# Kernel tuning notes

Hardware: AMD Instinct MI355X
Metric: run time of the kernel (lower is better)

Reference implementation:

```python
import jax, jax.numpy as jnp
import numpy as np

NUM_NODES = 100000
EMBED_DIM = 64
NUM_EDGES = 1200000
NUM_LAYERS = 3
ALPHA = 0.25  # 1 / (num_layers + 1)


def setup_inputs() -> dict:
    key = jax.random.key(0)
    k1, k2, k3, k4 = jax.random.split(key, 4)
    x = jax.random.normal(k1, (NUM_NODES, EMBED_DIM), dtype=jnp.float32)
    edge_attr = jax.random.uniform(k2, (NUM_EDGES,), dtype=jnp.float32)
    edge_index = jax.random.randint(k3, (2, NUM_EDGES), 0, NUM_NODES, dtype=jnp.int64)
    edge_mask = jax.random.randint(k4, (NUM_EDGES,), 0, 2, dtype=jnp.int32).astype(jnp.bool_)
    return {"x": x, "edge_attr": edge_attr, "edge_index": edge_index, "edge_mask": edge_mask}


def reference(x, edge_attr, edge_index, edge_mask):
    # Masked edge selection == zeroing masked edge weights (same degree & aggregation).
    w = edge_attr * edge_mask.astype(edge_attr.dtype)  # [E]
    row, col = edge_index[0], edge_index[1]            # source, target

    # gcn_norm with add_self_loops=False: D^{-1/2} A D^{-1/2}
    deg = jax.ops.segment_sum(w, col, num_segments=NUM_NODES)          # [N]
    dinv = jnp.where(deg > 0, jax.lax.rsqrt(deg), 0.0)                 # [N]
    norm = dinv[row] * w * dinv[col]                                   # [E]

    out = ALPHA * x
    h = x
    for _ in range(NUM_LAYERS):
        msg = norm[:, None] * h[row]                                   # [E, D] gather
        h = jax.ops.segment_sum(msg, col, num_segments=NUM_NODES)      # [N, D] scatter
        out = out + ALPHA * h
    return out
```

## Files before the change

kernel.cpp:

```cpp
#include <hip/hip_runtime.h>
#include <hip/hip_fp16.h>

#define N_NODES 100000
#define EMB     64
#define N_EDGES 1200000
#define ALPHA   0.25f
#define SCAN_CHUNK 1024
#define NPART ((N_NODES + SCAN_CHUNK - 1) / SCAN_CHUNK)

__global__ void k_detect(const unsigned char* __restrict__ maskB,
                         const int* __restrict__ idx, int* __restrict__ flags) {
    int tid = blockIdx.x * blockDim.x + threadIdx.x;
    int lane = threadIdx.x & 63;
    bool mev = (tid & 3) && maskB[tid];
    if (__any(mev) && lane == 0) atomicOr(&flags[0], 1);
    bool iev = (tid < 4096) && (idx[2 * tid + 1] != 0);
    if (__any(iev) && lane == 0) atomicOr(&flags[1], 1);
}

__device__ __forceinline__ int idx_row(const int* idx, int i64, int e) {
    return i64 ? idx[2 * e] : idx[e];
}
__device__ __forceinline__ int idx_col(const int* idx, int i64, int e) {
    return i64 ? idx[2 * (N_EDGES + e)] : idx[N_EDGES + e];
}
__device__ __forceinline__ int edge_mask(const void* maskp, int mbool, int e) {
    return mbool ? (int)((const unsigned char*)maskp)[e] : ((const int*)maskp)[e];
}

__global__ void k_hist(const float* __restrict__ ea, const void* maskp,
                       const int* __restrict__ idx, const int* __restrict__ flags,
                       int* __restrict__ cnt, int* __restrict__ rank) {
    int e = blockIdx.x * blockDim.x + threadIdx.x;
    if (e >= N_EDGES) return;
    int mbool = flags[0] != 0, i64 = (flags[1] == 0);
    if (!edge_mask(maskp, mbool, e)) return;
    float wv = ea[e];
    if (wv == 0.0f) return;
    int c = idx_col(idx, i64, e);
    if ((unsigned)c >= N_NODES) return;
    rank[e] = atomicAdd(&cnt[c], 1);
}

__global__ void k_scanx(const int* __restrict__ cnt, int* __restrict__ gTotal,
                        int* __restrict__ row_start) {
    __shared__ int sh[256];
    __shared__ int sbase;
    int tid = threadIdx.x;
    int base = blockIdx.x * SCAN_CHUNK + tid * 4;
    int v[4];
    int s = 0;
#pragma unroll
    for (int k = 0; k < 4; ++k) {
        int i = base + k;
        v[k] = (i < N_NODES) ? cnt[i] : 0;
        s += v[k];
    }
    sh[tid] = s;
    __syncthreads();
    for (int d = 1; d < 256; d <<= 1) {
        int t = (tid >= d) ? sh[tid - d] : 0;
        __syncthreads();
        sh[tid] += t;
        __syncthreads();
    }
    if (tid == 255) sbase = atomicAdd(gTotal, sh[255]);
    __syncthreads();
    int off = sbase + sh[tid] - s;
#pragma unroll
    for (int k = 0; k < 4; ++k) {
        int i = base + k;
        if (i < N_NODES) { row_start[i] = off; off += v[k]; }
    }
}

__global__ void k_fill(const float* __restrict__ ea, const void* maskp,
                       const int* __restrict__ idx, const int* __restrict__ flags,
                       const int* __restrict__ row_start, const int* __restrict__ rank,
                       int2* __restrict__ csr) {
    int e = blockIdx.x * blockDim.x + threadIdx.x;
    if (e >= N_EDGES) return;
    int mbool = flags[0] != 0, i64 = (flags[1] == 0);
    if (!edge_mask(maskp, mbool, e)) return;
    float wv = ea[e];
    if (wv == 0.0f) return;
    int c = idx_col(idx, i64, e);
    if ((unsigned)c >= N_NODES) return;
    int r = idx_row(idx, i64, e);
    int rok = (unsigned)r < N_NODES;
    int p = row_start[c] + rank[e];
    if ((unsigned)p < N_EDGES)
        csr[p] = make_int2(__float_as_int(rok ? wv : 0.0f), rok ? r : 0);
}

__device__ __forceinline__ void slice_bounds(const int* row_start, const int* cnt,
                                             int n, int& beg, int& end) {
    beg = row_start[n];
    if (beg < 0) beg = 0;
    if (beg > N_EDGES) beg = N_EDGES;
    int c = cnt[n];
    if (c < 0) c = 0;
    end = beg + c;
    if (end > N_EDGES) end = N_EDGES;
}

__global__ __launch_bounds__(256) void k_degconv(
        const int* __restrict__ row_start, const int* __restrict__ cnt,
        const int2* __restrict__ csr, const float4* __restrict__ x4,
        float4* __restrict__ t0, float* __restrict__ dinv, float* __restrict__ sd) {
    int t = blockIdx.x * blockDim.x + threadIdx.x;
    int n = t >> 3;
    int q = t & 7;
    if (n >= N_NODES) return;
    int beg, end;
    slice_bounds(row_start, cnt, n, beg, end);
    float s = 0.0f;
    for (int j = beg + q; j < end; j += 8) s += __int_as_float(csr[j].x);
    s += __shfl_xor(s, 1);
    s += __shfl_xor(s, 2);
    s += __shfl_xor(s, 4);
    float di = (s > 0.0f) ? rsqrtf(s) : 0.0f;
    if (q == 0) {
        dinv[n] = di;
        sd[n] = (s > 0.0f) ? sqrtf(s) : 0.0f;
    }
    size_t xb = (size_t)n * 16 + q * 2;
    float4 v0 = x4[xb], v1 = x4[xb + 1];
    float4 o;
    __half2* op = reinterpret_cast<__half2*>(&o);
    op[0] = __floats2half2_rn(di * v0.x, di * v0.y);
    op[1] = __floats2half2_rn(di * v0.z, di * v0.w);
    op[2] = __floats2half2_rn(di * v1.x, di * v1.y);
    op[3] = __floats2half2_rn(di * v1.z, di * v1.w);
    t0[(size_t)n * 8 + q] = o;
}

__device__ __forceinline__ void accum_h8(float4& sa, float4& sb, float w,
                                         float4 raw) {
    const __half2* hp = reinterpret_cast<const __half2*>(&raw);
    float2 f0 = __half22float2(hp[0]);
    float2 f1 = __half22float2(hp[1]);
    float2 f2 = __half22float2(hp[2]);
    float2 f3 = __half22float2(hp[3]);
    sa.x += w * f0.x; sa.y += w * f0.y; sa.z += w * f1.x; sa.w += w * f1.y;
    sb.x += w * f2.x; sb.y += w * f2.y; sb.z += w * f3.x; sb.w += w * f3.y;
}

__device__ __forceinline__ void gather_core_f16(
        const int* __restrict__ row_start, const int* __restrict__ cnt,
        const int2* __restrict__ csr, const float4* __restrict__ h16,
        int n, int q, float4& sa, float4& sb) {
    int beg, end;
    slice_bounds(row_start, cnt, n, beg, end);
    sa = make_float4(0.f, 0.f, 0.f, 0.f);
    sb = make_float4(0.f, 0.f, 0.f, 0.f);
    for (int j = beg; j < end; j += 4) {
        int last = end - 1;
        int j1 = j + 1 < last ? j + 1 : last;
        int j2 = j + 2 < last ? j + 2 : last;
        int j3 = j + 3 < last ? j + 3 : last;
        int2 p0 = csr[j];
        int2 p1 = csr[j1];
        int2 p2 = csr[j2];
        int2 p3 = csr[j3];
        bool a1 = j + 1 < end, a2 = j + 2 < end, a3 = j + 3 < end;
        float w0 = __int_as_float(p0.x);
        float w1 = a1 ? __int_as_float(p1.x) : 0.0f;
        float w2 = a2 ? __int_as_float(p2.x) : 0.0f;
        float w3 = a3 ? __int_as_float(p3.x) : 0.0f;
        int r0 = min((unsigned)p0.y, (unsigned)(N_NODES - 1));
        int r1 = a1 ? min((unsigned)p1.y, (unsigned)(N_NODES - 1)) : 0;
        int r2 = a2 ? min((unsigned)p2.y, (unsigned)(N_NODES - 1)) : 0;
        int r3 = a3 ? min((unsigned)p3.y, (unsigned)(N_NODES - 1)) : 0;
        float4 v0 = h16[(size_t)r0 * 8 + q];
        float4 v1 = h16[(size_t)r1 * 8 + q];
        float4 v2 = h16[(size_t)r2 * 8 + q];
        float4 v3 = h16[(size_t)r3 * 8 + q];
        accum_h8(sa, sb, w0, v0);
        accum_h8(sa, sb, w1, v1);
        accum_h8(sa, sb, w2, v2);
        accum_h8(sa, sb, w3, v3);
    }
}

__global__ __launch_bounds__(256) void k_gather_mid(
        const int* __restrict__ row_start, const int* __restrict__ cnt,
        const int2* __restrict__ csr, const float* __restrict__ dinv,
        const float4* __restrict__ tsrc, float4* __restrict__ tdst) {
    int t = blockIdx.x * blockDim.x + threadIdx.x;
    int n = t >> 3;
    int q = t & 7;
    if (n >= N_NODES) return;
    float4 sa, sb;
    gather_core_f16(row_start, cnt, csr, tsrc, n, q, sa, sb);
    float di = dinv[n];
    float d2 = di * di;
    float4 o;
    __half2* op = reinterpret_cast<__half2*>(&o);
    op[0] = __floats2half2_rn(d2 * sa.x, d2 * sa.y);
    op[1] = __floats2half2_rn(d2 * sa.z, d2 * sa.w);
    op[2] = __floats2half2_rn(d2 * sb.x, d2 * sb.y);
    op[3] = __floats2half2_rn(d2 * sb.z, d2 * sb.w);
    tdst[(size_t)n * 8 + q] = o;
}

__global__ __launch_bounds__(256) void k_gather_last(
        const int* __restrict__ row_start, const int* __restrict__ cnt,
        const int2* __restrict__ csr, const float* __restrict__ dinv,
        const float* __restrict__ sd,
        const float4* __restrict__ x4, const float4* __restrict__ t1_16,
        const float4* __restrict__ t2_16, float4* __restrict__ out4) {
    int t = blockIdx.x * blockDim.x + threadIdx.x;
    int n = t >> 3;
    int q = t & 7;
    if (n >= N_NODES) return;
    float4 sa, sb;
    gather_core_f16(row_start, cnt, csr, t2_16, n, q, sa, sb);
    float di = dinv[n];
    float sdv = sd[n];
    size_t o8 = (size_t)n * 8 + q;
    float4 r1 = t1_16[o8];
    float4 r2 = t2_16[o8];
    const __half2* a1 = reinterpret_cast<const __half2*>(&r1);
    const __half2* a2 = reinterpret_cast<const __half2*>(&r2);
    float2 b10 = __half22float2(a1[0]), b11 = __half22float2(a1[1]);
    float2 b12 = __half22float2(a1[2]), b13 = __half22float2(a1[3]);
    float2 b20 = __half22float2(a2[0]), b21 = __half22float2(a2[1]);
    float2 b22 = __half22float2(a2[2]), b23 = __half22float2(a2[3]);
    size_t ox = (size_t)n * 16 + 2 * q;
    float4 x0 = x4[ox], x1 = x4[ox + 1];
    float4 o0, o1;
    o0.x = ALPHA * (x0.x + sdv * (b10.x + b20.x) + di * sa.x);
    o0.y = ALPHA * (x0.y + sdv * (b10.y + b20.y) + di * sa.y);
    o0.z = ALPHA * (x0.z + sdv * (b11.x + b21.x) + di * sa.z);
    o0.w = ALPHA * (x0.w + sdv * (b11.y + b21.y) + di * sa.w);
    o1.x = ALPHA * (x1.x + sdv * (b12.x + b22.x) + di * sb.x);
    o1.y = ALPHA * (x1.y + sdv * (b12.y + b22.y) + di * sb.y);
    o1.z = ALPHA * (x1.z + sdv * (b13.x + b23.x) + di * sb.z);
    o1.w = ALPHA * (x1.w + sdv * (b13.y + b23.y) + di * sb.w);
    out4[ox] = o0;
    out4[ox + 1] = o1;
}

extern "C" void kernel_launch(void* const* d_in, const int* in_sizes, int n_in,
                              void* d_out, int out_size, void* d_ws, size_t ws_size,
                              hipStream_t stream) {
    const float* x   = (const float*)d_in[0];
    const float* ea  = (const float*)d_in[1];
    const int*   idx = (const int*)d_in[2];
    const void*  msk = d_in[3];
    float*       out = (float*)d_out;

    char* ws = (char*)d_ws;
    size_t off = 0;
    auto alloc = [&](size_t bytes) -> void* {
        void* p = ws + off;
        off = (off + bytes + 255) & ~(size_t)255;
        return p;
    };
    int*    flags     = (int*)   alloc(64);
    int*    cnt       = (int*)   alloc(sizeof(int)   * N_NODES);
    int*    row_start = (int*)   alloc(sizeof(int)   * N_NODES);
    float*  dinv      = (float*) alloc(sizeof(float) * N_NODES);
    float*  sd        = (float*) alloc(sizeof(float) * N_NODES);
    int*    rank      = (int*)   alloc(sizeof(int)   * N_EDGES);
    int2*   csr       = (int2*)  alloc(sizeof(int2)  * N_EDGES);
    float4* t0        = (float4*)alloc(sizeof(unsigned short) * (size_t)N_NODES * EMB);
    float4* tA        = (float4*)alloc(sizeof(unsigned short) * (size_t)N_NODES * EMB);
    float4* tB        = (float4*)alloc(sizeof(unsigned short) * (size_t)N_NODES * EMB);
    int*    gTotal    = flags + 8;

    const int B = 256;
    const int gE = (N_EDGES + B - 1) / B;
    const int gG = (N_NODES * 8 + B - 1) / B;

    (void)hipMemsetAsync(flags, 0, (size_t)((char*)row_start - (char*)flags), stream);
    k_detect <<<64, 256, 0, stream>>>((const unsigned char*)msk, idx, flags);
    k_hist   <<<gE, B, 0, stream>>>(ea, msk, idx, flags, cnt, rank);
    k_scanx  <<<NPART, 256, 0, stream>>>(cnt, gTotal, row_start);
    k_fill   <<<gE, B, 0, stream>>>(ea, msk, idx, flags, row_start, rank, csr);
    k_degconv<<<gG, B, 0, stream>>>(row_start, cnt, csr, (const float4*)x,
                                    t0, dinv, sd);

    k_gather_mid <<<gG, B, 0, stream>>>(row_start, cnt, csr, dinv, t0, tA);
    k_gather_mid <<<gG, B, 0, stream>>>(row_start, cnt, csr, dinv, tA, tB);
    k_gather_last<<<gG, B, 0, stream>>>(row_start, cnt, csr, dinv, sd,
                                        (const float4*)x, tA, tB, (float4*)out);
}
```

Measured before the change: 191.8 us.

## Replace per-edge rank array with atomic cursors and widen gather unroll to 8

The fill kernel now claims CSR slots with an atomic increment on a per-node cursor initialised by the scan. This removes the per-edge rank array write and read, and the histogram no longer returns atomic results. Zeroing of the count array moves from a memset into the detect kernel. The gather loop now loads 8 edges per iteration instead of 4 to keep more loads in flight. The cost is a second pass of contended atomics in fill, nondeterministic edge order within each row, and higher register pressure in the gather.

```diff
diff --git a/kernel.cpp b/kernel.cpp
--- a/kernel.cpp
+++ b/kernel.cpp
@@ -9,13 +9,15 @@
 #define NPART ((N_NODES + SCAN_CHUNK - 1) / SCAN_CHUNK)
 
 __global__ void k_detect(const unsigned char* __restrict__ maskB,
-                         const int* __restrict__ idx, int* __restrict__ flags) {
+                         const int* __restrict__ idx, int* __restrict__ flags,
+                         int* __restrict__ cnt) {
     int tid = blockIdx.x * blockDim.x + threadIdx.x;
     int lane = threadIdx.x & 63;
     bool mev = (tid & 3) && maskB[tid];
     if (__any(mev) && lane == 0) atomicOr(&flags[0], 1);
     bool iev = (tid < 4096) && (idx[2 * tid + 1] != 0);
     if (__any(iev) && lane == 0) atomicOr(&flags[1], 1);
+    for (int i = tid; i < N_NODES; i += 64 * 256) cnt[i] = 0;
 }
 
 __device__ __forceinline__ int idx_row(const int* idx, int i64, int e) {
@@ -30,7 +32,7 @@
 
 __global__ void k_hist(const float* __restrict__ ea, const void* maskp,
                        const int* __restrict__ idx, const int* __restrict__ flags,
-                       int* __restrict__ cnt, int* __restrict__ rank) {
+                       int* __restrict__ cnt) {
     int e = blockIdx.x * blockDim.x + threadIdx.x;
     if (e >= N_EDGES) return;
     int mbool = flags[0] != 0, i64 = (flags[1] == 0);
@@ -39,11 +41,11 @@
     if (wv == 0.0f) return;
     int c = idx_col(idx, i64, e);
     if ((unsigned)c >= N_NODES) return;
-    rank[e] = atomicAdd(&cnt[c], 1);
+    atomicAdd(&cnt[c], 1);
 }
 
 __global__ void k_scanx(const int* __restrict__ cnt, int* __restrict__ gTotal,
-                        int* __restrict__ row_start) {
+                        int* __restrict__ row_start, int* __restrict__ cursor) {
     __shared__ int sh[256];
     __shared__ int sbase;
     int tid = threadIdx.x;
@@ -70,14 +72,13 @@
 #pragma unroll
     for (int k = 0; k < 4; ++k) {
         int i = base + k;
-        if (i < N_NODES) { row_start[i] = off; off += v[k]; }
+        if (i < N_NODES) { row_start[i] = off; cursor[i] = off; off += v[k]; }
     }
 }
 
 __global__ void k_fill(const float* __restrict__ ea, const void* maskp,
                        const int* __restrict__ idx, const int* __restrict__ flags,
-                       const int* __restrict__ row_start, const int* __restrict__ rank,
-                       int2* __restrict__ csr) {
+                       int* __restrict__ cursor, int2* __restrict__ csr) {
     int e = blockIdx.x * blockDim.x + threadIdx.x;
     if (e >= N_EDGES) return;
     int mbool = flags[0] != 0, i64 = (flags[1] == 0);
@@ -88,7 +89,7 @@
     if ((unsigned)c >= N_NODES) return;
     int r = idx_row(idx, i64, e);
     int rok = (unsigned)r < N_NODES;
-    int p = row_start[c] + rank[e];
+    int p = atomicAdd(&cursor[c], 1);
     if ((unsigned)p < N_EDGES)
         csr[p] = make_int2(__float_as_int(rok ? wv : 0.0f), rok ? r : 0);
 }
@@ -154,32 +155,27 @@
     slice_bounds(row_start, cnt, n, beg, end);
     sa = make_float4(0.f, 0.f, 0.f, 0.f);
     sb = make_float4(0.f, 0.f, 0.f, 0.f);
-    for (int j = beg; j < end; j += 4) {
+    for (int j = beg; j < end; j += 8) {
         int last = end - 1;
-        int j1 = j + 1 < last ? j + 1 : last;
-        int j2 = j + 2 < last ? j + 2 : last;
-        int j3 = j + 3 < last ? j + 3 : last;
-        int2 p0 = csr[j];
-        int2 p1 = csr[j1];
-        int2 p2 = csr[j2];
-        int2 p3 = csr[j3];
-        bool a1 = j + 1 < end, a2 = j + 2 < end, a3 = j + 3 < end;
-        float w0 = __int_as_float(p0.x);
-        float w1 = a1 ? __int_as_float(p1.x) : 0.0f;
-        float w2 = a2 ? __int_as_float(p2.x) : 0.0f;
-        float w3 = a3 ? __int_as_float(p3.x) : 0.0f;
-        int r0 = min((unsigned)p0.y, (unsigned)(N_NODES - 1));
-        int r1 = a1 ? min((unsigned)p1.y, (unsigned)(N_NODES - 1)) : 0;
-        int r2 = a2 ? min((unsigned)p2.y, (unsigned)(N_NODES - 1)) : 0;
-        int r3 = a3 ? min((unsigned)p3.y, (unsigned)(N_NODES - 1)) : 0;
-        float4 v0 = h16[(size_t)r0 * 8 + q];
-        float4 v1 = h16[(size_t)r1 * 8 + q];
-        float4 v2 = h16[(size_t)r2 * 8 + q];
-        float4 v3 = h16[(size_t)r3 * 8 + q];
-        accum_h8(sa, sb, w0, v0);
-        accum_h8(sa, sb, w1, v1);
-        accum_h8(sa, sb, w2, v2);
-        accum_h8(sa, sb, w3, v3);
+        int2 p[8];
+#pragma unroll
+        for (int k = 0; k < 8; ++k) {
+            int jk = (j + k < last) ? j + k : last;
+            p[k] = csr[jk];
+        }
+        float w[8];
+        int   r[8];
+#pragma unroll
+        for (int k = 0; k < 8; ++k) {
+            bool ak = (j + k) < end;
+            w[k] = ak ? __int_as_float(p[k].x) : 0.0f;
+            r[k] = ak ? min((unsigned)p[k].y, (unsigned)(N_NODES - 1)) : 0;
+        }
+        float4 v[8];
+#pragma unroll
+        for (int k = 0; k < 8; ++k) v[k] = h16[(size_t)r[k] * 8 + q];
+#pragma unroll
+        for (int k = 0; k < 8; ++k) accum_h8(sa, sb, w[k], v[k]);
     }
 }
 
@@ -261,9 +257,9 @@
     int*    flags     = (int*)   alloc(64);
     int*    cnt       = (int*)   alloc(sizeof(int)   * N_NODES);
     int*    row_start = (int*)   alloc(sizeof(int)   * N_NODES);
+    int*    cursor    = (int*)   alloc(sizeof(int)   * N_NODES);
     float*  dinv      = (float*) alloc(sizeof(float) * N_NODES);
     float*  sd        = (float*) alloc(sizeof(float) * N_NODES);
-    int*    rank      = (int*)   alloc(sizeof(int)   * N_EDGES);
     int2*   csr       = (int2*)  alloc(sizeof(int2)  * N_EDGES);
     float4* t0        = (float4*)alloc(sizeof(unsigned short) * (size_t)N_NODES * EMB);
     float4* tA        = (float4*)alloc(sizeof(unsigned short) * (size_t)N_NODES * EMB);
@@ -274,11 +270,11 @@
     const int gE = (N_EDGES + B - 1) / B;
     const int gG = (N_NODES * 8 + B - 1) / B;
 
-    (void)hipMemsetAsync(flags, 0, (size_t)((char*)row_start - (char*)flags), stream);
-    k_detect <<<64, 256, 0, stream>>>((const unsigned char*)msk, idx, flags);
-    k_hist   <<<gE, B, 0, stream>>>(ea, msk, idx, flags, cnt, rank);
-    k_scanx  <<<NPART, 256, 0, stream>>>(cnt, gTotal, row_start);
-    k_fill   <<<gE, B, 0, stream>>>(ea, msk, idx, flags, row_start, rank, csr);
+    (void)hipMemsetAsync(flags, 0, 64, stream);
+    k_detect <<<64, 256, 0, stream>>>((const unsigned char*)msk, idx, flags, cnt);
+    k_hist   <<<gE, B, 0, stream>>>(ea, msk, idx, flags, cnt);
+    k_scanx  <<<NPART, 256, 0, stream>>>(cnt, gTotal, row_start, cursor);
+    k_fill   <<<gE, B, 0, stream>>>(ea, msk, idx, flags, cursor, csr);
     k_degconv<<<gG, B, 0, stream>>>(row_start, cnt, csr, (const float4*)x,
                                     t0, dinv, sd);
 
```

After: 216.2 us. +12.7%, slower.

## Pad CSR segments to multiples of four for aligned vector loads

Applied to the files above, without the earlier changes.

The scan now rounds each node's edge count up to a multiple of four and zero-fills the padding slots, so every segment starts 32-byte aligned. The gather loop then reads pairs of int4 with a one-step software prefetch, and drops the per-edge bounds clamping and validity predicates. The cost is a larger CSR buffer, extra zero-weight gathers of row 0 for padded slots, and removal of defensive clamping on row_start.

```diff
diff --git a/kernel.cpp b/kernel.cpp
--- a/kernel.cpp
+++ b/kernel.cpp
@@ -4,6 +4,7 @@
 #define N_NODES 100000
 #define EMB     64
 #define N_EDGES 1200000
+#define N_EPAD  (N_EDGES + 3 * N_NODES + 64)
 #define ALPHA   0.25f
 #define SCAN_CHUNK 1024
 #define NPART ((N_NODES + SCAN_CHUNK - 1) / SCAN_CHUNK)
@@ -43,18 +44,20 @@
 }
 
 __global__ void k_scanx(const int* __restrict__ cnt, int* __restrict__ gTotal,
-                        int* __restrict__ row_start) {
+                        int* __restrict__ row_start, int2* __restrict__ csr) {
     __shared__ int sh[256];
     __shared__ int sbase;
     int tid = threadIdx.x;
     int base = blockIdx.x * SCAN_CHUNK + tid * 4;
-    int v[4];
+    int v[4], p[4];
     int s = 0;
 #pragma unroll
     for (int k = 0; k < 4; ++k) {
         int i = base + k;
         v[k] = (i < N_NODES) ? cnt[i] : 0;
-        s += v[k];
+        if (v[k] < 0) v[k] = 0;
+        p[k] = (v[k] + 3) & ~3;
+        s += p[k];
     }
     sh[tid] = s;
     __syncthreads();
@@ -70,7 +73,12 @@
 #pragma unroll
     for (int k = 0; k < 4; ++k) {
         int i = base + k;
-        if (i < N_NODES) { row_start[i] = off; off += v[k]; }
+        if (i < N_NODES) {
+            row_start[i] = off;
+            for (int z = v[k]; z < p[k]; ++z)
+                if ((unsigned)(off + z) < N_EPAD) csr[off + z] = make_int2(0, 0);
+            off += p[k];
+        }
     }
 }
 
@@ -89,19 +97,8 @@
     int r = idx_row(idx, i64, e);
     int rok = (unsigned)r < N_NODES;
     int p = row_start[c] + rank[e];
-    if ((unsigned)p < N_EDGES)
+    if ((unsigned)p < N_EPAD)
         csr[p] = make_int2(__float_as_int(rok ? wv : 0.0f), rok ? r : 0);
-}
-
-__device__ __forceinline__ void slice_bounds(const int* row_start, const int* cnt,
-                                             int n, int& beg, int& end) {
-    beg = row_start[n];
-    if (beg < 0) beg = 0;
-    if (beg > N_EDGES) beg = N_EDGES;
-    int c = cnt[n];
-    if (c < 0) c = 0;
-    end = beg + c;
-    if (end > N_EDGES) end = N_EDGES;
 }
 
 __global__ __launch_bounds__(256) void k_degconv(
@@ -112,10 +109,12 @@
     int n = t >> 3;
     int q = t & 7;
     if (n >= N_NODES) return;
-    int beg, end;
-    slice_bounds(row_start, cnt, n, beg, end);
+    int beg = row_start[n];
+    int c = cnt[n];
+    if (c < 0) c = 0;
+    int pc = (c + 3) & ~3;
     float s = 0.0f;
-    for (int j = beg + q; j < end; j += 8) s += __int_as_float(csr[j].x);
+    for (int j = q; j < pc; j += 8) s += __int_as_float(csr[beg + j].x);
     s += __shfl_xor(s, 1);
     s += __shfl_xor(s, 2);
     s += __shfl_xor(s, 4);
@@ -150,28 +149,25 @@
         const int* __restrict__ row_start, const int* __restrict__ cnt,
         const int2* __restrict__ csr, const float4* __restrict__ h16,
         int n, int q, float4& sa, float4& sb) {
-    int beg, end;
-    slice_bounds(row_start, cnt, n, beg, end);
     sa = make_float4(0.f, 0.f, 0.f, 0.f);
     sb = make_float4(0.f, 0.f, 0.f, 0.f);
-    for (int j = beg; j < end; j += 4) {
-        int last = end - 1;
-        int j1 = j + 1 < last ? j + 1 : last;
-        int j2 = j + 2 < last ? j + 2 : last;
-        int j3 = j + 3 < last ? j + 3 : last;
-        int2 p0 = csr[j];
-        int2 p1 = csr[j1];
-        int2 p2 = csr[j2];
-        int2 p3 = csr[j3];
-        bool a1 = j + 1 < end, a2 = j + 2 < end, a3 = j + 3 < end;
-        float w0 = __int_as_float(p0.x);
-        float w1 = a1 ? __int_as_float(p1.x) : 0.0f;
-        float w2 = a2 ? __int_as_float(p2.x) : 0.0f;
-        float w3 = a3 ? __int_as_float(p3.x) : 0.0f;
-        int r0 = min((unsigned)p0.y, (unsigned)(N_NODES - 1));
-        int r1 = a1 ? min((unsigned)p1.y, (unsigned)(N_NODES - 1)) : 0;
-        int r2 = a2 ? min((unsigned)p2.y, (unsigned)(N_NODES - 1)) : 0;
-        int r3 = a3 ? min((unsigned)p3.y, (unsigned)(N_NODES - 1)) : 0;
+    int beg = row_start[n];
+    int c = cnt[n];
+    if (c <= 0) return;
+    int nb = ((c + 3) & ~3) >> 2;
+    const int4* csr4 = (const int4*)(csr + beg);
+    int4 a = csr4[0], b = csr4[1];
+    for (int t = 0; t < nb; ++t) {
+        int4 pa = a, pb = b;
+        if (t + 1 < nb) { a = csr4[2 * t + 2]; b = csr4[2 * t + 3]; }
+        float w0 = __int_as_float(pa.x);
+        float w1 = __int_as_float(pa.z);
+        float w2 = __int_as_float(pb.x);
+        float w3 = __int_as_float(pb.z);
+        int r0 = min((unsigned)pa.y, (unsigned)(N_NODES - 1));
+        int r1 = min((unsigned)pa.w, (unsigned)(N_NODES - 1));
+        int r2 = min((unsigned)pb.y, (unsigned)(N_NODES - 1));
+        int r3 = min((unsigned)pb.w, (unsigned)(N_NODES - 1));
         float4 v0 = h16[(size_t)r0 * 8 + q];
         float4 v1 = h16[(size_t)r1 * 8 + q];
         float4 v2 = h16[(size_t)r2 * 8 + q];
@@ -264,7 +260,7 @@
     float*  dinv      = (float*) alloc(sizeof(float) * N_NODES);
     float*  sd        = (float*) alloc(sizeof(float) * N_NODES);
     int*    rank      = (int*)   alloc(sizeof(int)   * N_EDGES);
-    int2*   csr       = (int2*)  alloc(sizeof(int2)  * N_EDGES);
+    int2*   csr       = (int2*)  alloc(sizeof(int2)  * N_EPAD);
     float4* t0        = (float4*)alloc(sizeof(unsigned short) * (size_t)N_NODES * EMB);
     float4* tA        = (float4*)alloc(sizeof(unsigned short) * (size_t)N_NODES * EMB);
     float4* tB        = (float4*)alloc(sizeof(unsigned short) * (size_t)N_NODES * EMB);
@@ -277,7 +273,7 @@
     (void)hipMemsetAsync(flags, 0, (size_t)((char*)row_start - (char*)flags), stream);
     k_detect <<<64, 256, 0, stream>>>((const unsigned char*)msk, idx, flags);
     k_hist   <<<gE, B, 0, stream>>>(ea, msk, idx, flags, cnt, rank);
-    k_scanx  <<<NPART, 256, 0, stream>>>(cnt, gTotal, row_start);
+    k_scanx  <<<NPART, 256, 0, stream>>>(cnt, gTotal, row_start, csr);
     k_fill   <<<gE, B, 0, stream>>>(ea, msk, idx, flags, row_start, rank, csr);
     k_degconv<<<gG, B, 0, stream>>>(row_start, cnt, csr, (const float4*)x,
                                     t0, dinv, sd);
```

Result: no change. 193.7 us (+1.0%).
